# Kernel tuning notes

Hardware: AMD Instinct MI355X
Metric: run time of the kernel (lower is better)

## Reference

```python
import jax, jax.numpy as jnp
import numpy as np

NUM_HEADS = 8
DIM_HEAD = 48
SCALE = DIM_HEAD ** -0.5


def setup_inputs() -> dict:
    key = jax.random.key(0)
    k1, k2, k3 = jax.random.split(key, 3)
    B, N, D = 4, 2048, 384
    inner = NUM_HEADS * DIM_HEAD  # 384
    x = jax.random.normal(k1, (B, N, D), dtype=jnp.float32)
    # store weights in [in, out] layout (equivalent to torch Linear W.T)
    Wqkv = jax.random.normal(k2, (D, 3 * inner), dtype=jnp.float32) * (D ** -0.5)
    Wproj = jax.random.normal(k3, (inner, D), dtype=jnp.float32) * (inner ** -0.5)
    bproj = jnp.zeros((D,), dtype=jnp.float32)
    return {"x": x, "Wqkv": Wqkv, "Wproj": Wproj, "bproj": bproj}


def reference(x, Wqkv, Wproj, bproj):
    B, N, D = x.shape
    h, dh = NUM_HEADS, DIM_HEAD
    C = h * dh
    # fused QKV projection (qkv_bias=False)
    qkv = (x @ Wqkv).reshape(B, N, 3, h, dh)
    q = qkv[:, :, 0].transpose(0, 2, 1, 3)  # [B, h, N, dh]
    k = qkv[:, :, 1].transpose(0, 2, 1, 3)
    v = qkv[:, :, 2].transpose(0, 2, 1, 3)
    # naive attention: materialize [B, h, N, N] scores
    sim = jnp.einsum("bhqd,bhkd->bhqk", q, k) * SCALE
    attn = jax.nn.softmax(sim, axis=-1)
    out = jnp.einsum("bhqk,bhkd->bhqd", attn, v)  # [B, h, N, dh]
    out = out.transpose(0, 2, 1, 3).reshape(B, N, C)
    return out @ Wproj + bproj
```

## Files before the change

### kernel.cpp

```cpp
#include <hip/hip_runtime.h>
#include <hip/hip_bf16.h>


typedef _Float16 f16x8 __attribute__((ext_vector_type(8)));
typedef _Float16 f16x4 __attribute__((ext_vector_type(4)));
typedef float    f32x4 __attribute__((ext_vector_type(4)));
typedef float    f32x16 __attribute__((ext_vector_type(16)));

#define QSCL 0.20822035963448658f

__global__ __launch_bounds__(256) void prep(const float4* __restrict__ x,
                                            const float* __restrict__ wq,
                                            const float* __restrict__ wp,
                                            f16x4* __restrict__ xh4,
                                            _Float16* __restrict__ wqt,
                                            _Float16* __restrict__ wpt)
{
    __shared__ _Float16 t[64][65];
    const int blk = blockIdx.x, tid = threadIdx.x;
    if (blk < 144) {
        const float* src; _Float16* dst; int Nn, k0, n0;
        if (blk < 108) {
            src = wq; dst = wqt; Nn = 1152;
            k0 = (blk % 6) * 64; n0 = (blk / 6) * 64;
        } else {
            const int b2 = blk - 108;
            src = wp; dst = wpt; Nn = 384;
            k0 = (b2 % 6) * 64; n0 = (b2 / 6) * 64;
        }
        #pragma unroll
        for (int i = 0; i < 16; i++) {
            const int id = tid + i * 256;
            const int k = id >> 6, n = id & 63;
            t[k][n] = (_Float16)src[(size_t)(k0 + k) * Nn + n0 + n];
        }
        __syncthreads();
        #pragma unroll
        for (int i = 0; i < 16; i++) {
            const int id = tid + i * 256;
            const int n = id >> 6, k = id & 63;
            dst[(size_t)(n0 + n) * 384 + k0 + k] = t[k][n];
        }
    } else {
        const int base = (blk - 144) * 3072;
        #pragma unroll
        for (int r = 0; r < 12; r++) {
            const int j = base + r * 256 + tid;
            const float4 tt = x[j];
            f16x4 hh;
            hh[0] = (_Float16)tt.x; hh[1] = (_Float16)tt.y;
            hh[2] = (_Float16)tt.z; hh[3] = (_Float16)tt.w;
            xh4[j] = hh;
        }
    }
}

union QkvSmem {
    struct { _Float16 As[128][40]; _Float16 Bs[128][40]; } g;
    _Float16 Ts[128][136];
    _Float16 Ts2[128][136];
};

__global__ __launch_bounds__(256) void qkv_f16(const _Float16* __restrict__ A,
                                               const _Float16* __restrict__ Bt,
                                               _Float16* __restrict__ qh,
                                               _Float16* __restrict__ kh,
                                               _Float16* __restrict__ vt)
{
    __shared__ QkvSmem sm;
    const int tid = threadIdx.x;
    const int w = tid >> 6, lane = tid & 63, cl = lane & 15, quad = lane >> 4;
    const int bm = blockIdx.x, bn = blockIdx.y;

    f32x4 acc[2][8];
    const f32x4 z4 = {0.f, 0.f, 0.f, 0.f};
    #pragma unroll
    for (int mi = 0; mi < 2; mi++)
        #pragma unroll
        for (int t = 0; t < 8; t++) acc[mi][t] = z4;

    const int ar = tid >> 2, ac = (tid & 3) * 8;
    const _Float16* Ag = A  + (size_t)(bm * 128 + ar) * 384 + ac;
    const _Float16* Bg = Bt + (size_t)(bn * 128 + ar) * 384 + ac;

    f16x8 pa[2], pb[2];
    #pragma unroll
    for (int j = 0; j < 2; j++) {
        pa[j] = *(const f16x8*)(Ag + (size_t)(64 * j) * 384);
        pb[j] = *(const f16x8*)(Bg + (size_t)(64 * j) * 384);
    }

    for (int k0 = 0; k0 < 384; k0 += 32) {
        __syncthreads();
        #pragma unroll
        for (int j = 0; j < 2; j++) {
            *(f16x8*)&sm.g.As[ar + 64 * j][ac] = pa[j];
            *(f16x8*)&sm.g.Bs[ar + 64 * j][ac] = pb[j];
        }
        __syncthreads();
        if (k0 + 32 < 384) {
            #pragma unroll
            for (int j = 0; j < 2; j++) {
                pa[j] = *(const f16x8*)(Ag + (size_t)(64 * j) * 384 + k0 + 32);
                pb[j] = *(const f16x8*)(Bg + (size_t)(64 * j) * 384 + k0 + 32);
            }
        }
        f16x8 bf[8];
        #pragma unroll
        for (int t = 0; t < 8; t++)
            bf[t] = *(const f16x8*)&sm.g.Bs[t * 16 + cl][quad * 8];
        #pragma unroll
        for (int mi = 0; mi < 2; mi++) {
            const f16x8 af = *(const f16x8*)&sm.g.As[w * 32 + mi * 16 + cl][quad * 8];
            #pragma unroll
            for (int t = 0; t < 8; t++)
                acc[mi][t] = __builtin_amdgcn_mfma_f32_16x16x32_f16(af, bf[t], acc[mi][t], 0, 0, 0);
        }
    }

    const int s = (bn * 128) / 384;
    const int b  = (bm * 128) >> 11;
    const int n0 = (bm * 128) & 2047;
    if (s == 2) {
        __syncthreads();
        #pragma unroll
        for (int t = 0; t < 8; t++)
            #pragma unroll
            for (int mi = 0; mi < 2; mi++)
                #pragma unroll
                for (int r = 0; r < 4; r++)
                    sm.Ts[t * 16 + cl][w * 32 + mi * 16 + quad * 4 + r] =
                        (_Float16)acc[mi][t][r];
        __syncthreads();
        const int colbase = bn * 128 - 768;
        #pragma unroll
        for (int i = 0; i < 8; i++) {
            const int c = i * 256 + tid;
            const int col = c >> 4, nc = c & 15;
            const int gcol = colbase + col;
            const int head = gcol / 48, d = gcol - head * 48;
            const int bh = b * 8 + head;
            *(f16x8*)&vt[(size_t)(bh * 48 + d) * 2048 + n0 + nc * 8] =
                *(const f16x8*)&sm.Ts[col][nc * 8];
        }
    } else {
        __syncthreads();
        const float scl = (s == 0) ? QSCL : 1.0f;
        #pragma unroll
        for (int t = 0; t < 8; t++)
            #pragma unroll
            for (int mi = 0; mi < 2; mi++)
                #pragma unroll
                for (int r = 0; r < 4; r++)
                    sm.Ts2[w * 32 + mi * 16 + quad * 4 + r][t * 16 + cl] =
                        (_Float16)(acc[mi][t][r] * scl);
        __syncthreads();
        _Float16* dst = (s == 0) ? qh : kh;
        const int colbase = bn * 128 - s * 384;
        #pragma unroll
        for (int i = 0; i < 8; i++) {
            const int c = i * 256 + tid;
            const int row = c >> 4, ch = c & 15;
            const int gcol = colbase + ch * 8;
            const int head = gcol / 48, d = gcol - head * 48;
            const int bh = b * 8 + head;
            *(f16x8*)&dst[(size_t)(bh * 2048 + n0 + row) * 48 + d] =
                *(const f16x8*)&sm.Ts2[row][ch * 8];
        }
    }
}

union AttnSmem {
    struct {
        _Float16 Ks[64][56];
        _Float16 Vts[64][72];
    } a;
    _Float16 Ot[128][58];
};

__global__ __launch_bounds__(256) void attn_f16(const _Float16* __restrict__ qh,
                                                const _Float16* __restrict__ kh,
                                                const _Float16* __restrict__ vt,
                                                _Float16* __restrict__ ab)
{
    __shared__ AttnSmem sm;
    const int tid = threadIdx.x;
    const int w = tid >> 6, lane = tid & 63, ln = lane & 31, h = lane >> 5;
    const int bh = blockIdx.x, qt = blockIdx.y;

    for (int i = tid; i < 16 * 72; i += 256) {
        const int r = 48 + i / 72, c = i - (i / 72) * 72;
        sm.a.Vts[r][c] = (r == 48) ? (_Float16)1.0f : (_Float16)0.0f;
    }

    f16x8 qf[3];
    {
        const _Float16* qp = qh + (size_t)(bh * 2048 + qt * 128 + w * 32 + ln) * 48 + 8 * h;
        qf[0] = *(const f16x8*)qp;
        qf[1] = *(const f16x8*)(qp + 16);
        qf[2] = *(const f16x8*)(qp + 32);
    }

    f32x16 o0, o1;
    #pragma unroll
    for (int r = 0; r < 16; r++) { o0[r] = 0.f; o1[r] = 0.f; }

    const _Float16* kbase = kh + (size_t)bh * 2048 * 48;
    const _Float16* vbase = vt + (size_t)bh * 48 * 2048;

    const int kr0 = tid / 6,         kc0 = (tid % 6) * 8;
    const int kid1 = tid + 256;
    const int kr1 = kid1 / 6,        kc1 = (kid1 % 6) * 8;
    const int vr0 = tid >> 3,        vc0 = (tid & 7) * 8;
    const int vr1 = (tid + 256) >> 3;
    const int vslot_lo = 16 * ((tid & 7) >> 1) + 4 * (tid & 1);
    const _Float16* ks0 = kbase + (size_t)kr0 * 48 + kc0;
    const _Float16* ks1 = kbase + (size_t)kr1 * 48 + kc1;
    const _Float16* vs0 = vbase + (size_t)vr0 * 2048 + vc0;
    const _Float16* vs1 = vbase + (size_t)vr1 * 2048 + vc0;

    f16x8 rk0 = *(const f16x8*)ks0;
    f16x8 rv0 = *(const f16x8*)vs0;
    f16x8 rk1, rv1;
    if (tid < 128) { rk1 = *(const f16x8*)ks1; rv1 = *(const f16x8*)vs1; }

    for (int kt = 0; kt < 2048; kt += 64) {
        __syncthreads();
        *(f16x8*)&sm.a.Ks[kr0][kc0] = rk0;
        {
            const f16x4* rvh = (const f16x4*)&rv0;
            *(f16x4*)&sm.a.Vts[vr0][vslot_lo]     = rvh[0];
            *(f16x4*)&sm.a.Vts[vr0][vslot_lo + 8] = rvh[1];
        }
        if (tid < 128) {
            *(f16x8*)&sm.a.Ks[kr1][kc1] = rk1;
            const f16x4* rvh = (const f16x4*)&rv1;
            *(f16x4*)&sm.a.Vts[vr1][vslot_lo]     = rvh[0];
            *(f16x4*)&sm.a.Vts[vr1][vslot_lo + 8] = rvh[1];
        }
        __syncthreads();
        if (kt + 64 < 2048) {
            rk0 = *(const f16x8*)(ks0 + (size_t)(kt + 64) * 48);
            rv0 = *(const f16x8*)(vs0 + kt + 64);
            if (tid < 128) {
                rk1 = *(const f16x8*)(ks1 + (size_t)(kt + 64) * 48);
                rv1 = *(const f16x8*)(vs1 + kt + 64);
            }
        }

        f32x16 s0, s1;
        #pragma unroll
        for (int r = 0; r < 16; r++) { s0[r] = 0.f; s1[r] = 0.f; }
        #pragma unroll
        for (int i = 0; i < 3; i++) {
            const f16x8 ka0 = *(const f16x8*)&sm.a.Ks[ln][16 * i + 8 * h];
            s0 = __builtin_amdgcn_mfma_f32_32x32x16_f16(ka0, qf[i], s0, 0, 0, 0);
            const f16x8 ka1 = *(const f16x8*)&sm.a.Ks[32 + ln][16 * i + 8 * h];
            s1 = __builtin_amdgcn_mfma_f32_32x32x16_f16(ka1, qf[i], s1, 0, 0, 0);
        }

        f16x8 pbf[4];
        #pragma unroll
        for (int j = 0; j < 8; j++) {
            pbf[0][j] = (_Float16)exp2f(s0[j]);
            pbf[1][j] = (_Float16)exp2f(s0[8 + j]);
            pbf[2][j] = (_Float16)exp2f(s1[j]);
            pbf[3][j] = (_Float16)exp2f(s1[8 + j]);
        }

        #pragma unroll
        for (int c = 0; c < 4; c++) {
            const f16x8 av0 = *(const f16x8*)&sm.a.Vts[ln][16 * c + 8 * h];
            o0 = __builtin_amdgcn_mfma_f32_32x32x16_f16(av0, pbf[c], o0, 0, 0, 0);
            const f16x8 av1 = *(const f16x8*)&sm.a.Vts[32 + ln][16 * c + 8 * h];
            o1 = __builtin_amdgcn_mfma_f32_32x32x16_f16(av1, pbf[c], o1, 0, 0, 0);
        }
    }

    const float lr  = __shfl(o1[8], ln);
    const float inv = 1.f / lr;

    __syncthreads();
    #pragma unroll
    for (int r = 0; r < 16; r++)
        sm.Ot[w * 32 + ln][(r & 3) + 8 * (r >> 2) + 4 * h] = (_Float16)(o0[r] * inv);
    #pragma unroll
    for (int r = 0; r < 8; r++)
        sm.Ot[w * 32 + ln][32 + (r & 3) + 8 * (r >> 2) + 4 * h] = (_Float16)(o1[r] * inv);
    __syncthreads();
    const int b = bh >> 3, hd = bh & 7;
    #pragma unroll
    for (int i = 0; i < 3; i++) {
        const int c2 = i * 256 + tid;
        const int row = c2 / 6, ch = c2 % 6;
        const int q = qt * 128 + row;
        *(f16x8*)&ab[(size_t)(b * 2048 + q) * 384 + hd * 48 + ch * 8] =
            *(const f16x8*)&sm.Ot[row][ch * 8];
    }
}

__global__ __launch_bounds__(256) void proj_f16(const _Float16* __restrict__ A,
                                                const _Float16* __restrict__ Bt,
                                                const float* __restrict__ bias,
                                                float* __restrict__ out)
{
    __shared__ _Float16 As[64][72];
    __shared__ _Float16 Bs[64][72];
    const int tid = threadIdx.x;
    const int w = tid >> 6, lane = tid & 63, cl = lane & 15, quad = lane >> 4;
    const int bm = blockIdx.x, bn = blockIdx.y;

    f32x4 acc[4];
    const f32x4 z4 = {0.f, 0.f, 0.f, 0.f};
    #pragma unroll
    for (int t = 0; t < 4; t++) acc[t] = z4;

    const int ar = tid >> 3, ac = (tid & 7) * 8;
    const _Float16* Ag = A  + (size_t)(bm * 64 + ar) * 384 + ac;
    const _Float16* Bg = Bt + (size_t)(bn * 64 + ar) * 384 + ac;

    f16x8 pa[2], pb[2];
    #pragma unroll
    for (int j = 0; j < 2; j++) {
        pa[j] = *(const f16x8*)(Ag + (size_t)(32 * j) * 384);
        pb[j] = *(const f16x8*)(Bg + (size_t)(32 * j) * 384);
    }

    for (int k0 = 0; k0 < 384; k0 += 64) {
        __syncthreads();
        #pragma unroll
        for (int j = 0; j < 2; j++) {
            *(f16x8*)&As[ar + 32 * j][ac] = pa[j];
            *(f16x8*)&Bs[ar + 32 * j][ac] = pb[j];
        }
        __syncthreads();
        if (k0 + 64 < 384) {
            #pragma unroll
            for (int j = 0; j < 2; j++) {
                pa[j] = *(const f16x8*)(Ag + (size_t)(32 * j) * 384 + k0 + 64);
                pb[j] = *(const f16x8*)(Bg + (size_t)(32 * j) * 384 + k0 + 64);
            }
        }
        #pragma unroll
        for (int kh2 = 0; kh2 < 2; kh2++) {
            const f16x8 af = *(const f16x8*)&As[w * 16 + cl][kh2 * 32 + quad * 8];
            #pragma unroll
            for (int t = 0; t < 4; t++) {
                const f16x8 bf = *(const f16x8*)&Bs[t * 16 + cl][kh2 * 32 + quad * 8];
                acc[t] = __builtin_amdgcn_mfma_f32_16x16x32_f16(af, bf, acc[t], 0, 0, 0);
            }
        }
    }

    #pragma unroll
    for (int t = 0; t < 4; t++) {
        const int col = bn * 64 + t * 16 + cl;
        const float bv = bias[col];
        #pragma unroll
        for (int r = 0; r < 4; r++) {
            const int row = bm * 64 + w * 16 + quad * 4 + r;
            out[(size_t)row * 384 + col] = acc[t][r] + bv;
        }
    }
}

extern "C" void kernel_launch(void* const* d_in, const int* in_sizes, int n_in,
                              void* d_out, int out_size, void* d_ws, size_t ws_size,
                              hipStream_t stream) {
    const float* x     = (const float*)d_in[0];
    const float* Wqkv  = (const float*)d_in[1];
    const float* Wproj = (const float*)d_in[2];
    const float* bproj = (const float*)d_in[3];
    float* out = (float*)d_out;

    char* ws = (char*)d_ws;
    _Float16* xh     = (_Float16*)(ws + 0);
    _Float16* wqkvt  = (_Float16*)(ws + 6291456);
    _Float16* wprojt = (_Float16*)(ws + 7176192);
    _Float16* qh     = (_Float16*)(ws + 7471104);
    _Float16* kh     = (_Float16*)(ws + 13762560);
    _Float16* vt     = (_Float16*)(ws + 20054016);
    _Float16* ab     = (_Float16*)(ws + 26345472);

    prep<<<400, 256, 0, stream>>>((const float4*)x, Wqkv, Wproj,
                                  (f16x4*)xh, wqkvt, wprojt);
    qkv_f16<<<dim3(64, 9), 256, 0, stream>>>(xh, wqkvt, qh, kh, vt);
    attn_f16<<<dim3(32, 16), 256, 0, stream>>>(qh, kh, vt, ab);
    proj_f16<<<dim3(128, 6), 256, 0, stream>>>(ab, wprojt, bproj, out);
}
```

Baseline: 146.8 us.

## Split attention KV range across two blocks and add combine kernel

Splits each attention tile's key/value sequence into two halves processed by separate blocks (grid z=2). Each block writes unnormalized fp32 partial outputs and row sums, and a new combine kernel adds them and normalizes into fp16. It also double-buffers the K/V shared tiles to drop one barrier per iteration and raises wave priority around MFMA sections. The aim is more blocks to fill the GPU (512 to 1024), at the cost of extra fp32 partial traffic and an additional kernel launch.

```diff
diff --git a/kernel.cpp b/kernel.cpp
--- a/kernel.cpp
+++ b/kernel.cpp
@@ -172,25 +172,27 @@
 
 union AttnSmem {
     struct {
-        _Float16 Ks[64][56];
-        _Float16 Vts[64][72];
+        _Float16 Ks[2][64][56];
+        _Float16 Vts[2][64][72];
     } a;
-    _Float16 Ot[128][58];
+    float Otf[128][52];
 };
 
 __global__ __launch_bounds__(256) void attn_f16(const _Float16* __restrict__ qh,
                                                 const _Float16* __restrict__ kh,
                                                 const _Float16* __restrict__ vt,
-                                                _Float16* __restrict__ ab)
+                                                float* __restrict__ opart,
+                                                float* __restrict__ lpart)
 {
     __shared__ AttnSmem sm;
     const int tid = threadIdx.x;
     const int w = tid >> 6, lane = tid & 63, ln = lane & 31, h = lane >> 5;
-    const int bh = blockIdx.x, qt = blockIdx.y;
-
-    for (int i = tid; i < 16 * 72; i += 256) {
-        const int r = 48 + i / 72, c = i - (i / 72) * 72;
-        sm.a.Vts[r][c] = (r == 48) ? (_Float16)1.0f : (_Float16)0.0f;
+    const int bh = blockIdx.x, qt = blockIdx.y, sp = blockIdx.z;
+
+    for (int i = tid; i < 2 * 16 * 72; i += 256) {
+        const int bi = i / (16 * 72), j = i - bi * (16 * 72);
+        const int r = 48 + j / 72, c = j - (j / 72) * 72;
+        sm.a.Vts[bi][r][c] = (r == 48) ? (_Float16)1.0f : (_Float16)0.0f;
     }
 
     f16x8 qf[3];
@@ -205,8 +207,8 @@
     #pragma unroll
     for (int r = 0; r < 16; r++) { o0[r] = 0.f; o1[r] = 0.f; }
 
-    const _Float16* kbase = kh + (size_t)bh * 2048 * 48;
-    const _Float16* vbase = vt + (size_t)bh * 48 * 2048;
+    const _Float16* kbase = kh + (size_t)bh * 2048 * 48 + (size_t)sp * 1024 * 48;
+    const _Float16* vbase = vt + (size_t)bh * 48 * 2048 + sp * 1024;
 
     const int kr0 = tid / 6,         kc0 = (tid % 6) * 8;
     const int kid1 = tid + 256;
@@ -224,40 +226,46 @@
     f16x8 rk1, rv1;
     if (tid < 128) { rk1 = *(const f16x8*)ks1; rv1 = *(const f16x8*)vs1; }
 
-    for (int kt = 0; kt < 2048; kt += 64) {
-        __syncthreads();
-        *(f16x8*)&sm.a.Ks[kr0][kc0] = rk0;
+    for (int t = 0; t < 16; ++t) {
+        _Float16 (*Ksb)[56] = sm.a.Ks[t & 1];
+        _Float16 (*Vtb)[72] = sm.a.Vts[t & 1];
+
+        *(f16x8*)&Ksb[kr0][kc0] = rk0;
         {
             const f16x4* rvh = (const f16x4*)&rv0;
-            *(f16x4*)&sm.a.Vts[vr0][vslot_lo]     = rvh[0];
-            *(f16x4*)&sm.a.Vts[vr0][vslot_lo + 8] = rvh[1];
+            *(f16x4*)&Vtb[vr0][vslot_lo]     = rvh[0];
+            *(f16x4*)&Vtb[vr0][vslot_lo + 8] = rvh[1];
         }
         if (tid < 128) {
-            *(f16x8*)&sm.a.Ks[kr1][kc1] = rk1;
+            *(f16x8*)&Ksb[kr1][kc1] = rk1;
             const f16x4* rvh = (const f16x4*)&rv1;
-            *(f16x4*)&sm.a.Vts[vr1][vslot_lo]     = rvh[0];
-            *(f16x4*)&sm.a.Vts[vr1][vslot_lo + 8] = rvh[1];
-        }
-        __syncthreads();
-        if (kt + 64 < 2048) {
-            rk0 = *(const f16x8*)(ks0 + (size_t)(kt + 64) * 48);
-            rv0 = *(const f16x8*)(vs0 + kt + 64);
+            *(f16x4*)&Vtb[vr1][vslot_lo]     = rvh[0];
+            *(f16x4*)&Vtb[vr1][vslot_lo + 8] = rvh[1];
+        }
+        __syncthreads();
+
+        if (t < 15) {
+            const int off = (t + 1) * 64;
+            rk0 = *(const f16x8*)(ks0 + (size_t)off * 48);
+            rv0 = *(const f16x8*)(vs0 + off);
             if (tid < 128) {
-                rk1 = *(const f16x8*)(ks1 + (size_t)(kt + 64) * 48);
-                rv1 = *(const f16x8*)(vs1 + kt + 64);
+                rk1 = *(const f16x8*)(ks1 + (size_t)off * 48);
+                rv1 = *(const f16x8*)(vs1 + off);
             }
         }
 
         f32x16 s0, s1;
         #pragma unroll
         for (int r = 0; r < 16; r++) { s0[r] = 0.f; s1[r] = 0.f; }
+        __builtin_amdgcn_s_setprio(1);
         #pragma unroll
         for (int i = 0; i < 3; i++) {
-            const f16x8 ka0 = *(const f16x8*)&sm.a.Ks[ln][16 * i + 8 * h];
+            const f16x8 ka0 = *(const f16x8*)&Ksb[ln][16 * i + 8 * h];
             s0 = __builtin_amdgcn_mfma_f32_32x32x16_f16(ka0, qf[i], s0, 0, 0, 0);
-            const f16x8 ka1 = *(const f16x8*)&sm.a.Ks[32 + ln][16 * i + 8 * h];
+            const f16x8 ka1 = *(const f16x8*)&Ksb[32 + ln][16 * i + 8 * h];
             s1 = __builtin_amdgcn_mfma_f32_32x32x16_f16(ka1, qf[i], s1, 0, 0, 0);
         }
+        __builtin_amdgcn_s_setprio(0);
 
         f16x8 pbf[4];
         #pragma unroll
@@ -268,35 +276,64 @@
             pbf[3][j] = (_Float16)exp2f(s1[8 + j]);
         }
 
+        __builtin_amdgcn_s_setprio(1);
         #pragma unroll
         for (int c = 0; c < 4; c++) {
-            const f16x8 av0 = *(const f16x8*)&sm.a.Vts[ln][16 * c + 8 * h];
+            const f16x8 av0 = *(const f16x8*)&Vtb[ln][16 * c + 8 * h];
             o0 = __builtin_amdgcn_mfma_f32_32x32x16_f16(av0, pbf[c], o0, 0, 0, 0);
-            const f16x8 av1 = *(const f16x8*)&sm.a.Vts[32 + ln][16 * c + 8 * h];
+            const f16x8 av1 = *(const f16x8*)&Vtb[32 + ln][16 * c + 8 * h];
             o1 = __builtin_amdgcn_mfma_f32_32x32x16_f16(av1, pbf[c], o1, 0, 0, 0);
         }
-    }
-
-    const float lr  = __shfl(o1[8], ln);
-    const float inv = 1.f / lr;
+        __builtin_amdgcn_s_setprio(0);
+    }
+
+    if (h == 0)
+        lpart[((size_t)sp * 32 + bh) * 2048 + qt * 128 + w * 32 + ln] = o1[8];
 
     __syncthreads();
     #pragma unroll
     for (int r = 0; r < 16; r++)
-        sm.Ot[w * 32 + ln][(r & 3) + 8 * (r >> 2) + 4 * h] = (_Float16)(o0[r] * inv);
+        sm.Otf[w * 32 + ln][(r & 3) + 8 * (r >> 2) + 4 * h] = o0[r];
     #pragma unroll
     for (int r = 0; r < 8; r++)
-        sm.Ot[w * 32 + ln][32 + (r & 3) + 8 * (r >> 2) + 4 * h] = (_Float16)(o1[r] * inv);
+        sm.Otf[w * 32 + ln][32 + (r & 3) + 8 * (r >> 2) + 4 * h] = o1[r];
     __syncthreads();
     const int b = bh >> 3, hd = bh & 7;
     #pragma unroll
-    for (int i = 0; i < 3; i++) {
+    for (int i = 0; i < 6; i++) {
         const int c2 = i * 256 + tid;
-        const int row = c2 / 6, ch = c2 % 6;
+        const int row = c2 / 12, ch = c2 % 12;
         const int q = qt * 128 + row;
-        *(f16x8*)&ab[(size_t)(b * 2048 + q) * 384 + hd * 48 + ch * 8] =
-            *(const f16x8*)&sm.Ot[row][ch * 8];
-    }
+        *(f32x4*)&opart[((size_t)sp * 8192 + b * 2048 + q) * 384 + hd * 48 + ch * 4] =
+            *(const f32x4*)&sm.Otf[row][ch * 4];
+    }
+}
+
+__global__ __launch_bounds__(256) void comb(const float* __restrict__ opart,
+                                            const float* __restrict__ lpart,
+                                            _Float16* __restrict__ ab)
+{
+    const int c = blockIdx.x * 256 + threadIdx.x;
+    const int row = c / 48, ch = c - row * 48;
+    const int b = row >> 11, q = row & 2047;
+    const int hd = ch / 6;
+    const size_t SP = (size_t)8192 * 384;
+    const float* p0 = opart + (size_t)row * 384 + ch * 8;
+    const f32x4 a0 = *(const f32x4*)p0;
+    const f32x4 a1 = *(const f32x4*)(p0 + 4);
+    const f32x4 b0 = *(const f32x4*)(p0 + SP);
+    const f32x4 b1 = *(const f32x4*)(p0 + SP + 4);
+    const int bh = b * 8 + hd;
+    const float l0 = lpart[(size_t)bh * 2048 + q];
+    const float l1 = lpart[(size_t)(32 + bh) * 2048 + q];
+    const float inv = 1.f / (l0 + l1);
+    f16x8 o;
+    #pragma unroll
+    for (int j = 0; j < 4; j++) {
+        o[j]     = (_Float16)((a0[j] + b0[j]) * inv);
+        o[4 + j] = (_Float16)((a1[j] + b1[j]) * inv);
+    }
+    *(f16x8*)&ab[(size_t)row * 384 + ch * 8] = o;
 }
 
 __global__ __launch_bounds__(256) void proj_f16(const _Float16* __restrict__ A,
@@ -374,17 +411,20 @@
     float* out = (float*)d_out;
 
     char* ws = (char*)d_ws;
-    _Float16* xh     = (_Float16*)(ws + 0);
-    _Float16* wqkvt  = (_Float16*)(ws + 6291456);
-    _Float16* wprojt = (_Float16*)(ws + 7176192);
-    _Float16* qh     = (_Float16*)(ws + 7471104);
-    _Float16* kh     = (_Float16*)(ws + 13762560);
-    _Float16* vt     = (_Float16*)(ws + 20054016);
-    _Float16* ab     = (_Float16*)(ws + 26345472);
+    _Float16* qh     = (_Float16*)(ws + 0);
+    _Float16* kh     = (_Float16*)(ws + 6291456);
+    _Float16* vt     = (_Float16*)(ws + 12582912);
+    _Float16* ab     = (_Float16*)(ws + 18874368);
+    _Float16* wprojt = (_Float16*)(ws + 25165824);
+    float*    lpart  = (float*)   (ws + 25460736);
+    float*    opart  = (float*)   (ws + 25985024);
+    _Float16* xh     = (_Float16*)(ws + 25985024);
+    _Float16* wqkvt  = (_Float16*)(ws + 32276480);
 
     prep<<<400, 256, 0, stream>>>((const float4*)x, Wqkv, Wproj,
                                   (f16x4*)xh, wqkvt, wprojt);
     qkv_f16<<<dim3(64, 9), 256, 0, stream>>>(xh, wqkvt, qh, kh, vt);
-    attn_f16<<<dim3(32, 16), 256, 0, stream>>>(qh, kh, vt, ab);
+    attn_f16<<<dim3(32, 16, 2), 256, 0, stream>>>(qh, kh, vt, opart, lpart);
+    comb<<<1536, 256, 0, stream>>>(opart, lpart, ab);
     proj_f16<<<dim3(128, 6), 256, 0, stream>>>(ab, wprojt, bproj, out);
 }
```

Result: slower. 157.7 us (+7.5%).

## Load K/V fragments directly from global into registers in attention, drop LDS staging

Applied to the files above, without the earlier changes.

The attention kernel no longer stages K and V tiles through shared memory with block-wide barriers. Each wave now loads its MFMA operand fragments straight from global memory into registers and prefetches the next tile while computing. The V layout written by the QKV kernel is permuted so these direct loads match the MFMA operand order. The softmax denominator is now a running sum of the exponentials instead of a ones-row in V. The change also adds s_setprio around the MFMA blocks and switches to the hardware exp2 builtin. It trades LDS traffic and barriers for redundant global/L2 loads, since every wave re-reads the same K/V.

```diff
diff --git a/kernel.cpp b/kernel.cpp
--- a/kernel.cpp
+++ b/kernel.cpp
@@ -123,13 +123,14 @@
     const int n0 = (bm * 128) & 2047;
     if (s == 2) {
         __syncthreads();
+        const int qp = ((quad & 1) << 1) | (quad >> 1);
         #pragma unroll
         for (int t = 0; t < 8; t++)
             #pragma unroll
             for (int mi = 0; mi < 2; mi++)
                 #pragma unroll
                 for (int r = 0; r < 4; r++)
-                    sm.Ts[t * 16 + cl][w * 32 + mi * 16 + quad * 4 + r] =
+                    sm.Ts[t * 16 + cl][w * 32 + mi * 16 + qp * 4 + r] =
                         (_Float16)acc[mi][t][r];
         __syncthreads();
         const int colbase = bn * 128 - 768;
@@ -170,28 +171,15 @@
     }
 }
 
-union AttnSmem {
-    struct {
-        _Float16 Ks[64][56];
-        _Float16 Vts[64][72];
-    } a;
-    _Float16 Ot[128][58];
-};
-
 __global__ __launch_bounds__(256) void attn_f16(const _Float16* __restrict__ qh,
                                                 const _Float16* __restrict__ kh,
                                                 const _Float16* __restrict__ vt,
                                                 _Float16* __restrict__ ab)
 {
-    __shared__ AttnSmem sm;
+    __shared__ _Float16 Ot[128][58];
     const int tid = threadIdx.x;
     const int w = tid >> 6, lane = tid & 63, ln = lane & 31, h = lane >> 5;
     const int bh = blockIdx.x, qt = blockIdx.y;
-
-    for (int i = tid; i < 16 * 72; i += 256) {
-        const int r = 48 + i / 72, c = i - (i / 72) * 72;
-        sm.a.Vts[r][c] = (r == 48) ? (_Float16)1.0f : (_Float16)0.0f;
-    }
 
     f16x8 qf[3];
     {
@@ -204,89 +192,84 @@
     f32x16 o0, o1;
     #pragma unroll
     for (int r = 0; r < 16; r++) { o0[r] = 0.f; o1[r] = 0.f; }
-
-    const _Float16* kbase = kh + (size_t)bh * 2048 * 48;
-    const _Float16* vbase = vt + (size_t)bh * 48 * 2048;
-
-    const int kr0 = tid / 6,         kc0 = (tid % 6) * 8;
-    const int kid1 = tid + 256;
-    const int kr1 = kid1 / 6,        kc1 = (kid1 % 6) * 8;
-    const int vr0 = tid >> 3,        vc0 = (tid & 7) * 8;
-    const int vr1 = (tid + 256) >> 3;
-    const int vslot_lo = 16 * ((tid & 7) >> 1) + 4 * (tid & 1);
-    const _Float16* ks0 = kbase + (size_t)kr0 * 48 + kc0;
-    const _Float16* ks1 = kbase + (size_t)kr1 * 48 + kc1;
-    const _Float16* vs0 = vbase + (size_t)vr0 * 2048 + vc0;
-    const _Float16* vs1 = vbase + (size_t)vr1 * 2048 + vc0;
-
-    f16x8 rk0 = *(const f16x8*)ks0;
-    f16x8 rv0 = *(const f16x8*)vs0;
-    f16x8 rk1, rv1;
-    if (tid < 128) { rk1 = *(const f16x8*)ks1; rv1 = *(const f16x8*)vs1; }
-
-    for (int kt = 0; kt < 2048; kt += 64) {
-        __syncthreads();
-        *(f16x8*)&sm.a.Ks[kr0][kc0] = rk0;
-        {
-            const f16x4* rvh = (const f16x4*)&rv0;
-            *(f16x4*)&sm.a.Vts[vr0][vslot_lo]     = rvh[0];
-            *(f16x4*)&sm.a.Vts[vr0][vslot_lo + 8] = rvh[1];
-        }
-        if (tid < 128) {
-            *(f16x8*)&sm.a.Ks[kr1][kc1] = rk1;
-            const f16x4* rvh = (const f16x4*)&rv1;
-            *(f16x4*)&sm.a.Vts[vr1][vslot_lo]     = rvh[0];
-            *(f16x4*)&sm.a.Vts[vr1][vslot_lo + 8] = rvh[1];
-        }
-        __syncthreads();
-        if (kt + 64 < 2048) {
-            rk0 = *(const f16x8*)(ks0 + (size_t)(kt + 64) * 48);
-            rv0 = *(const f16x8*)(vs0 + kt + 64);
-            if (tid < 128) {
-                rk1 = *(const f16x8*)(ks1 + (size_t)(kt + 64) * 48);
-                rv1 = *(const f16x8*)(vs1 + kt + 64);
-            }
-        }
+    float lsum = 0.f;
+
+    const _Float16* kp  = kh + ((size_t)bh * 2048 + ln) * 48 + 8 * h;
+    const int vrow1 = min(bh * 48 + 32 + ln, 32 * 48 - 1);
+    const _Float16* vp0 = vt + ((size_t)bh * 48 + ln) * 2048 + 8 * h;
+    const _Float16* vp1 = vt + (size_t)vrow1 * 2048 + 8 * h;
+
+    f16x8 kf[6], vf[8];
+    #pragma unroll
+    for (int i = 0; i < 3; i++) {
+        kf[i]     = *(const f16x8*)(kp + 16 * i);
+        kf[3 + i] = *(const f16x8*)(kp + (size_t)32 * 48 + 16 * i);
+    }
+    #pragma unroll
+    for (int c = 0; c < 4; c++) {
+        vf[c]     = *(const f16x8*)(vp0 + 16 * c);
+        vf[4 + c] = *(const f16x8*)(vp1 + 16 * c);
+    }
+
+    for (int t = 0; t < 32; ++t) {
+        const int nxt = ((t + 1) & 31) * 64;
 
         f32x16 s0, s1;
         #pragma unroll
         for (int r = 0; r < 16; r++) { s0[r] = 0.f; s1[r] = 0.f; }
+        __builtin_amdgcn_s_setprio(1);
         #pragma unroll
         for (int i = 0; i < 3; i++) {
-            const f16x8 ka0 = *(const f16x8*)&sm.a.Ks[ln][16 * i + 8 * h];
-            s0 = __builtin_amdgcn_mfma_f32_32x32x16_f16(ka0, qf[i], s0, 0, 0, 0);
-            const f16x8 ka1 = *(const f16x8*)&sm.a.Ks[32 + ln][16 * i + 8 * h];
-            s1 = __builtin_amdgcn_mfma_f32_32x32x16_f16(ka1, qf[i], s1, 0, 0, 0);
+            s0 = __builtin_amdgcn_mfma_f32_32x32x16_f16(kf[i],     qf[i], s0, 0, 0, 0);
+            s1 = __builtin_amdgcn_mfma_f32_32x32x16_f16(kf[3 + i], qf[i], s1, 0, 0, 0);
+        }
+        __builtin_amdgcn_s_setprio(0);
+
+        #pragma unroll
+        for (int i = 0; i < 3; i++) {
+            kf[i]     = *(const f16x8*)(kp + (size_t)nxt * 48 + 16 * i);
+            kf[3 + i] = *(const f16x8*)(kp + (size_t)(nxt + 32) * 48 + 16 * i);
         }
 
         f16x8 pbf[4];
+        float ls0 = 0.f, ls1 = 0.f, ls2 = 0.f, ls3 = 0.f;
         #pragma unroll
         for (int j = 0; j < 8; j++) {
-            pbf[0][j] = (_Float16)exp2f(s0[j]);
-            pbf[1][j] = (_Float16)exp2f(s0[8 + j]);
-            pbf[2][j] = (_Float16)exp2f(s1[j]);
-            pbf[3][j] = (_Float16)exp2f(s1[8 + j]);
-        }
-
+            const float e0 = __builtin_amdgcn_exp2f(s0[j]);
+            const float e1 = __builtin_amdgcn_exp2f(s0[8 + j]);
+            const float e2 = __builtin_amdgcn_exp2f(s1[j]);
+            const float e3 = __builtin_amdgcn_exp2f(s1[8 + j]);
+            ls0 += e0; ls1 += e1; ls2 += e2; ls3 += e3;
+            pbf[0][j] = (_Float16)e0;
+            pbf[1][j] = (_Float16)e1;
+            pbf[2][j] = (_Float16)e2;
+            pbf[3][j] = (_Float16)e3;
+        }
+        lsum += (ls0 + ls1) + (ls2 + ls3);
+
+        __builtin_amdgcn_s_setprio(1);
         #pragma unroll
         for (int c = 0; c < 4; c++) {
-            const f16x8 av0 = *(const f16x8*)&sm.a.Vts[ln][16 * c + 8 * h];
-            o0 = __builtin_amdgcn_mfma_f32_32x32x16_f16(av0, pbf[c], o0, 0, 0, 0);
-            const f16x8 av1 = *(const f16x8*)&sm.a.Vts[32 + ln][16 * c + 8 * h];
-            o1 = __builtin_amdgcn_mfma_f32_32x32x16_f16(av1, pbf[c], o1, 0, 0, 0);
-        }
-    }
-
-    const float lr  = __shfl(o1[8], ln);
-    const float inv = 1.f / lr;
-
-    __syncthreads();
+            o0 = __builtin_amdgcn_mfma_f32_32x32x16_f16(vf[c],     pbf[c], o0, 0, 0, 0);
+            o1 = __builtin_amdgcn_mfma_f32_32x32x16_f16(vf[4 + c], pbf[c], o1, 0, 0, 0);
+        }
+        __builtin_amdgcn_s_setprio(0);
+
+        #pragma unroll
+        for (int c = 0; c < 4; c++) {
+            vf[c]     = *(const f16x8*)(vp0 + nxt + 16 * c);
+            vf[4 + c] = *(const f16x8*)(vp1 + nxt + 16 * c);
+        }
+    }
+
+    const float inv = 1.f / (lsum + __shfl_xor(lsum, 32));
+
     #pragma unroll
     for (int r = 0; r < 16; r++)
-        sm.Ot[w * 32 + ln][(r & 3) + 8 * (r >> 2) + 4 * h] = (_Float16)(o0[r] * inv);
+        Ot[w * 32 + ln][(r & 3) + 8 * (r >> 2) + 4 * h] = (_Float16)(o0[r] * inv);
     #pragma unroll
     for (int r = 0; r < 8; r++)
-        sm.Ot[w * 32 + ln][32 + (r & 3) + 8 * (r >> 2) + 4 * h] = (_Float16)(o1[r] * inv);
+        Ot[w * 32 + ln][32 + (r & 3) + 8 * (r >> 2) + 4 * h] = (_Float16)(o1[r] * inv);
     __syncthreads();
     const int b = bh >> 3, hd = bh & 7;
     #pragma unroll
@@ -295,7 +278,7 @@
         const int row = c2 / 6, ch = c2 % 6;
         const int q = qt * 128 + row;
         *(f16x8*)&ab[(size_t)(b * 2048 + q) * 384 + hd * 48 + ch * 8] =
-            *(const f16x8*)&sm.Ot[row][ch * 8];
+            *(const f16x8*)&Ot[row][ch * 8];
     }
 }
 
```

Result: slower. 167.2 us (+13.9%).

## Double-buffer K/V tiles in attention, single barrier per step, packed exp conversion

Applied to the files above, without the earlier changes.

Makes the K and V shared-memory tiles double-buffered so each key step needs only one barrier instead of two. The V column permutation moves from the per-tile smem store into the QKV kernel's V-transpose write, so the attention kernel stores V with one 16-byte write. It also uses raw hardware exp2 with packed f16 conversion, and raises wave priority around the MFMA blocks. This trades about double the LDS footprint, which may reduce occupancy, for less synchronisation and fewer instructions per tile. Dropping the exp2f wrapper relies on inputs staying in range.

```diff
diff --git a/kernel.cpp b/kernel.cpp
--- a/kernel.cpp
+++ b/kernel.cpp
@@ -4,10 +4,15 @@
 
 typedef _Float16 f16x8 __attribute__((ext_vector_type(8)));
 typedef _Float16 f16x4 __attribute__((ext_vector_type(4)));
+typedef _Float16 f16x2 __attribute__((ext_vector_type(2)));
 typedef float    f32x4 __attribute__((ext_vector_type(4)));
 typedef float    f32x16 __attribute__((ext_vector_type(16)));
 
 #define QSCL 0.20822035963448658f
+
+static __device__ __forceinline__ f16x2 cvt_pk_f16(float a, float b) {
+    return __builtin_bit_cast(f16x2, __builtin_amdgcn_cvt_pkrtz(a, b));
+}
 
 __global__ __launch_bounds__(256) void prep(const float4* __restrict__ x,
                                             const float* __restrict__ wq,
@@ -123,13 +128,14 @@
     const int n0 = (bm * 128) & 2047;
     if (s == 2) {
         __syncthreads();
+        const int qp = ((quad & 1) << 1) | (quad >> 1);
         #pragma unroll
         for (int t = 0; t < 8; t++)
             #pragma unroll
             for (int mi = 0; mi < 2; mi++)
                 #pragma unroll
                 for (int r = 0; r < 4; r++)
-                    sm.Ts[t * 16 + cl][w * 32 + mi * 16 + quad * 4 + r] =
+                    sm.Ts[t * 16 + cl][w * 32 + mi * 16 + qp * 4 + r] =
                         (_Float16)acc[mi][t][r];
         __syncthreads();
         const int colbase = bn * 128 - 768;
@@ -170,10 +176,13 @@
     }
 }
 
+#define KS_S 58
+#define VS_S 74
+
 union AttnSmem {
     struct {
-        _Float16 Ks[64][56];
-        _Float16 Vts[64][72];
+        _Float16 Ks[2][64][KS_S];
+        _Float16 Vts[2][64][VS_S];
     } a;
     _Float16 Ot[128][58];
 };
@@ -188,9 +197,10 @@
     const int w = tid >> 6, lane = tid & 63, ln = lane & 31, h = lane >> 5;
     const int bh = blockIdx.x, qt = blockIdx.y;
 
-    for (int i = tid; i < 16 * 72; i += 256) {
-        const int r = 48 + i / 72, c = i - (i / 72) * 72;
-        sm.a.Vts[r][c] = (r == 48) ? (_Float16)1.0f : (_Float16)0.0f;
+    for (int i = tid; i < 2 * 16 * VS_S; i += 256) {
+        const int bi = i / (16 * VS_S), j = i - bi * (16 * VS_S);
+        const int r = 48 + j / VS_S, c = j - (j / VS_S) * VS_S;
+        sm.a.Vts[bi][r][c] = (r == 48) ? (_Float16)1.0f : (_Float16)0.0f;
     }
 
     f16x8 qf[3];
@@ -208,12 +218,11 @@
     const _Float16* kbase = kh + (size_t)bh * 2048 * 48;
     const _Float16* vbase = vt + (size_t)bh * 48 * 2048;
 
-    const int kr0 = tid / 6,         kc0 = (tid % 6) * 8;
+    const int kr0 = tid / 6,        kc0 = (tid % 6) * 8;
     const int kid1 = tid + 256;
-    const int kr1 = kid1 / 6,        kc1 = (kid1 % 6) * 8;
-    const int vr0 = tid >> 3,        vc0 = (tid & 7) * 8;
-    const int vr1 = (tid + 256) >> 3;
-    const int vslot_lo = 16 * ((tid & 7) >> 1) + 4 * (tid & 1);
+    const int kr1 = kid1 / 6,       kc1 = (kid1 % 6) * 8;
+    const int vr0 = tid >> 3,       vc0 = (tid & 7) * 8;
+    const int vr1 = vr0 + 32;
     const _Float16* ks0 = kbase + (size_t)kr0 * 48 + kc0;
     const _Float16* ks1 = kbase + (size_t)kr1 * 48 + kc1;
     const _Float16* vs0 = vbase + (size_t)vr0 * 2048 + vc0;
@@ -224,57 +233,64 @@
     f16x8 rk1, rv1;
     if (tid < 128) { rk1 = *(const f16x8*)ks1; rv1 = *(const f16x8*)vs1; }
 
-    for (int kt = 0; kt < 2048; kt += 64) {
-        __syncthreads();
-        *(f16x8*)&sm.a.Ks[kr0][kc0] = rk0;
-        {
-            const f16x4* rvh = (const f16x4*)&rv0;
-            *(f16x4*)&sm.a.Vts[vr0][vslot_lo]     = rvh[0];
-            *(f16x4*)&sm.a.Vts[vr0][vslot_lo + 8] = rvh[1];
-        }
+    for (int t = 0; t < 32; ++t) {
+        _Float16 (*Ksb)[KS_S] = sm.a.Ks[t & 1];
+        _Float16 (*Vtb)[VS_S] = sm.a.Vts[t & 1];
+
+        *(f16x8*)&Ksb[kr0][kc0] = rk0;
+        *(f16x8*)&Vtb[vr0][vc0] = rv0;
         if (tid < 128) {
-            *(f16x8*)&sm.a.Ks[kr1][kc1] = rk1;
-            const f16x4* rvh = (const f16x4*)&rv1;
-            *(f16x4*)&sm.a.Vts[vr1][vslot_lo]     = rvh[0];
-            *(f16x4*)&sm.a.Vts[vr1][vslot_lo + 8] = rvh[1];
-        }
-        __syncthreads();
-        if (kt + 64 < 2048) {
-            rk0 = *(const f16x8*)(ks0 + (size_t)(kt + 64) * 48);
-            rv0 = *(const f16x8*)(vs0 + kt + 64);
+            *(f16x8*)&Ksb[kr1][kc1] = rk1;
+            *(f16x8*)&Vtb[vr1][vc0] = rv1;
+        }
+        __syncthreads();
+
+        if (t < 31) {
+            const int off = (t + 1) * 64;
+            rk0 = *(const f16x8*)(ks0 + (size_t)off * 48);
+            rv0 = *(const f16x8*)(vs0 + off);
             if (tid < 128) {
-                rk1 = *(const f16x8*)(ks1 + (size_t)(kt + 64) * 48);
-                rv1 = *(const f16x8*)(vs1 + kt + 64);
+                rk1 = *(const f16x8*)(ks1 + (size_t)off * 48);
+                rv1 = *(const f16x8*)(vs1 + off);
             }
         }
 
         f32x16 s0, s1;
         #pragma unroll
         for (int r = 0; r < 16; r++) { s0[r] = 0.f; s1[r] = 0.f; }
+        __builtin_amdgcn_s_setprio(1);
         #pragma unroll
         for (int i = 0; i < 3; i++) {
-            const f16x8 ka0 = *(const f16x8*)&sm.a.Ks[ln][16 * i + 8 * h];
+            const f16x8 ka0 = *(const f16x8*)&Ksb[ln][16 * i + 8 * h];
             s0 = __builtin_amdgcn_mfma_f32_32x32x16_f16(ka0, qf[i], s0, 0, 0, 0);
-            const f16x8 ka1 = *(const f16x8*)&sm.a.Ks[32 + ln][16 * i + 8 * h];
+            const f16x8 ka1 = *(const f16x8*)&Ksb[32 + ln][16 * i + 8 * h];
             s1 = __builtin_amdgcn_mfma_f32_32x32x16_f16(ka1, qf[i], s1, 0, 0, 0);
         }
+        __builtin_amdgcn_s_setprio(0);
 
         f16x8 pbf[4];
-        #pragma unroll
-        for (int j = 0; j < 8; j++) {
-            pbf[0][j] = (_Float16)exp2f(s0[j]);
-            pbf[1][j] = (_Float16)exp2f(s0[8 + j]);
-            pbf[2][j] = (_Float16)exp2f(s1[j]);
-            pbf[3][j] = (_Float16)exp2f(s1[8 + j]);
-        }
-
+        f16x2* pp = (f16x2*)pbf;
+        #pragma unroll
+        for (int m = 0; m < 4; m++) {
+            pp[m]      = cvt_pk_f16(
+                __builtin_amdgcn_exp2f(s0[2 * m]),     __builtin_amdgcn_exp2f(s0[2 * m + 1]));
+            pp[4 + m]  = cvt_pk_f16(
+                __builtin_amdgcn_exp2f(s0[8 + 2 * m]), __builtin_amdgcn_exp2f(s0[9 + 2 * m]));
+            pp[8 + m]  = cvt_pk_f16(
+                __builtin_amdgcn_exp2f(s1[2 * m]),     __builtin_amdgcn_exp2f(s1[2 * m + 1]));
+            pp[12 + m] = cvt_pk_f16(
+                __builtin_amdgcn_exp2f(s1[8 + 2 * m]), __builtin_amdgcn_exp2f(s1[9 + 2 * m]));
+        }
+
+        __builtin_amdgcn_s_setprio(1);
         #pragma unroll
         for (int c = 0; c < 4; c++) {
-            const f16x8 av0 = *(const f16x8*)&sm.a.Vts[ln][16 * c + 8 * h];
+            const f16x8 av0 = *(const f16x8*)&Vtb[ln][16 * c + 8 * h];
             o0 = __builtin_amdgcn_mfma_f32_32x32x16_f16(av0, pbf[c], o0, 0, 0, 0);
-            const f16x8 av1 = *(const f16x8*)&sm.a.Vts[32 + ln][16 * c + 8 * h];
+            const f16x8 av1 = *(const f16x8*)&Vtb[32 + ln][16 * c + 8 * h];
             o1 = __builtin_amdgcn_mfma_f32_32x32x16_f16(av1, pbf[c], o1, 0, 0, 0);
         }
+        __builtin_amdgcn_s_setprio(0);
     }
 
     const float lr  = __shfl(o1[8], ln);
```

Result: slower. 217.1 us (+47.9%).
